# Optimization experiments

Hardware: AMD Instinct MI355X
Metric: run time of the kernel (lower is better)

Reference implementation:

```python
import jax, jax.numpy as jnp
import numpy as np

D, B, N, DIM, H, DH, MLP = 6, 4, 1024, 768, 12, 64, 3072
SCALE = DH ** -0.5
EPS = 1e-5


def setup_inputs() -> dict:
    key = jax.random.key(0)
    ks = jax.random.split(key, 5)
    s = 0.02
    return {
        "x": jax.random.normal(ks[0], (B, N, DIM), jnp.float32),
        "ln1_g": jnp.ones((D, DIM), jnp.float32),
        "ln1_b": jnp.zeros((D, DIM), jnp.float32),
        "wqkv": jax.random.normal(ks[1], (D, DIM, 3 * H * DH), jnp.float32) * s,
        "wo": jax.random.normal(ks[2], (D, H * DH, DIM), jnp.float32) * s,
        "bo": jnp.zeros((D, DIM), jnp.float32),
        "ln2_g": jnp.ones((D, DIM), jnp.float32),
        "ln2_b": jnp.zeros((D, DIM), jnp.float32),
        "w1": jax.random.normal(ks[3], (D, DIM, MLP), jnp.float32) * s,
        "b1": jnp.zeros((D, MLP), jnp.float32),
        "w2": jax.random.normal(ks[4], (D, MLP, DIM), jnp.float32) * s,
        "b2": jnp.zeros((D, DIM), jnp.float32),
    }


def _ln(h, g, b):
    m = h.mean(-1, keepdims=True)
    v = h.var(-1, keepdims=True)  # biased, matches torch LayerNorm
    return (h - m) / jnp.sqrt(v + EPS) * g + b


def _heads(t):
    # [b, n, h*d] -> [b, h, n, d]
    return t.reshape(B, N, H, DH).transpose(0, 2, 1, 3)


def reference(x, ln1_g, ln1_b, wqkv, wo, bo, ln2_g, ln2_b, w1, b1, w2, b2):
    def step(carry, p):
        xc, _, _ = carry
        g1, be1, Wqkv, Wo, Bo, g2, be2, W1, B1, W2, B2 = p
        h = _ln(xc, g1, be1)
        q, k, v = jnp.split(h @ Wqkv, 3, axis=-1)
        q, k, v = _heads(q), _heads(k), _heads(v)
        attn = jax.nn.softmax(jnp.einsum('bhid,bhjd->bhij', q, k) * SCALE, axis=-1)
        out = jnp.einsum('bhij,bhjd->bhid', attn, v)
        out = out.transpose(0, 2, 1, 3).reshape(B, N, H * DH)
        xc = xc + out @ Wo + Bo
        h2 = _ln(xc, g2, be2)
        xc = xc + jax.nn.gelu(h2 @ W1 + B1, approximate=False) @ W2 + B2
        return (xc, k, v), None

    kv0 = jnp.zeros((B, H, N, DH), x.dtype)
    (xf, k, v), _ = jax.lax.scan(
        step, (x, kv0, kv0),
        (ln1_g, ln1_b, wqkv, wo, bo, ln2_g, ln2_b, w1, b1, w2, b2))
    return xf, k, v
```

## Files before the change

### kernel.cpp

```cpp
#include <hip/hip_runtime.h>
#include <hip/hip_bf16.h>
#include <math.h>

typedef __bf16 bf16;
typedef __bf16 bf16x8 __attribute__((ext_vector_type(8)));
typedef float f32x4 __attribute__((ext_vector_type(4)));

enum { EPI_QKV = 0, EPI_GELU = 1 };

__device__ __forceinline__ void gload16(const void* g, void* s) {
  __builtin_amdgcn_global_load_lds((__attribute__((address_space(1))) void*)g,
                                   (__attribute__((address_space(3))) void*)s, 16, 0, 0);
}

#define MFMA16(a, b, c) __builtin_amdgcn_mfma_f32_16x16x32_bf16((a), (b), (c), 0, 0, 0)

__device__ __forceinline__ void xcd_swizzle(int& bx, int& by) {
  const int gx = gridDim.x, nwg = gx * gridDim.y;
  int bid = blockIdx.y * gx + blockIdx.x;
  if ((nwg & 7) == 0) bid = (bid & 7) * (nwg >> 3) + (bid >> 3);
  bx = bid % gx;
  by = bid / gx;
}

__global__ __launch_bounds__(256) void cast_x(const float* __restrict__ x,
                                              float* __restrict__ xq) {
  const int i = (blockIdx.x * 256 + threadIdx.x) * 4;
  float4 v = *(const float4*)(x + i);
  v.x = (float)(bf16)v.x; v.y = (float)(bf16)v.y;
  v.z = (float)(bf16)v.z; v.w = (float)(bf16)v.w;
  *(float4*)(xq + i) = v;
}

__global__ __launch_bounds__(256) void wconv_all(
    const float* __restrict__ wqkv, const float* __restrict__ wo,
    const float* __restrict__ w1, const float* __restrict__ w2,
    bf16* __restrict__ qkvT, bf16* __restrict__ woT,
    bf16* __restrict__ w1T, bf16* __restrict__ w2T, int lfix) {
  __shared__ float tile[64][65];
  const int bid = blockIdx.x, t = threadIdx.x;
  int l, r;
  if (lfix < 0) { l = bid / 1728; r = bid % 1728; } else { l = lfix; r = bid; }
  const int lo = (lfix < 0) ? l : 0;
  const float* W; bf16* Wt; int K, N, tt;
  if (r < 432)       { W = wqkv + (size_t)l * 768 * 2304; Wt = qkvT + (size_t)lo * 2304 * 768; K = 768;  N = 2304; tt = r; }
  else if (r < 576)  { W = wo   + (size_t)l * 768 * 768;  Wt = woT  + (size_t)lo * 768 * 768;  K = 768;  N = 768;  tt = r - 432; }
  else if (r < 1152) { W = w1   + (size_t)l * 768 * 3072; Wt = w1T  + (size_t)lo * 3072 * 768; K = 768;  N = 3072; tt = r - 576; }
  else               { W = w2   + (size_t)l * 3072 * 768; Wt = w2T  + (size_t)lo * 768 * 3072; K = 3072; N = 768;  tt = r - 1152; }
  const int ntx = N >> 6;
  const int n0 = (tt % ntx) * 64, k0 = (tt / ntx) * 64;
  const int tx = t & 63, ty = t >> 6;
#pragma unroll
  for (int rr = 0; rr < 16; ++rr) {
    const int row = ty + rr * 4;
    tile[row][tx] = W[(size_t)(k0 + row) * N + n0 + tx];
  }
  __syncthreads();
#pragma unroll
  for (int it = 0; it < 2; ++it) {
    const int c = it * 256 + t;
    const int n = c >> 3, kc = (c & 7) * 8;
    bf16x8 v;
#pragma unroll
    for (int j = 0; j < 8; ++j) v[j] = (bf16)tile[kc + j][n];
    *(bf16x8*)(Wt + (size_t)(n0 + n) * K + k0 + kc) = v;
  }
}

__global__ __launch_bounds__(256) void ln_kernel(const float* __restrict__ x,
                                                 const float* __restrict__ g,
                                                 const float* __restrict__ b,
                                                 bf16* __restrict__ out) {
  const int row = blockIdx.x, t = threadIdx.x;
  const float* xr = x + (size_t)row * 768;
  float v0 = xr[t], v1 = xr[t + 256], v2 = xr[t + 512];
  float s = v0 + v1 + v2, sq = v0 * v0 + v1 * v1 + v2 * v2;
#pragma unroll
  for (int m = 32; m; m >>= 1) { s += __shfl_xor(s, m); sq += __shfl_xor(sq, m); }
  __shared__ float rs[4], rq[4];
  const int w = t >> 6;
  if ((t & 63) == 0) { rs[w] = s; rq[w] = sq; }
  __syncthreads();
  s = rs[0] + rs[1] + rs[2] + rs[3];
  sq = rq[0] + rq[1] + rq[2] + rq[3];
  const float mean = s * (1.f / 768.f);
  const float var = sq * (1.f / 768.f) - mean * mean;
  const float rstd = rsqrtf(var + 1e-5f);
  bf16* orow = out + (size_t)row * 768;
  orow[t]       = (bf16)((v0 - mean) * rstd * g[t]       + b[t]);
  orow[t + 256] = (bf16)((v1 - mean) * rstd * g[t + 256] + b[t + 256]);
  orow[t + 512] = (bf16)((v2 - mean) * rstd * g[t + 512] + b[t + 512]);
}

template <int EPI>
__global__ __launch_bounds__(256) void gemm_s(
    const bf16* __restrict__ A, const bf16* __restrict__ Bt,
    const float* __restrict__ bias, bf16* __restrict__ Cb,
    bf16* __restrict__ qo, bf16* __restrict__ ko_, bf16* __restrict__ vo,
    float* __restrict__ kf, float* __restrict__ vf, int wf,
    int M, int Nc, int K) {
  __shared__ __align__(16) char lds[2][2][8192];
  const int t = threadIdx.x, lane = t & 63, w = t >> 6;
  const int wr = w >> 1, wc = w & 1;
  int bx, by;
  xcd_swizzle(bx, by);
  const size_t m0 = (size_t)by * 128, n0 = (size_t)bx * 128;

  const char* ab[2]; const char* bb[2];
#pragma unroll
  for (int r = 0; r < 2; ++r) {
    int c = r * 256 + t;
    ab[r] = (const char*)(A + (m0 + (c >> 2)) * (size_t)K) + (c & 3) * 16;
    bb[r] = (const char*)(Bt + (n0 + (c >> 2)) * (size_t)K) + (c & 3) * 16;
  }

  f32x4 acc[4][4] = {};

  auto stage = [&](int buf, int tt) {
#pragma unroll
    for (int r = 0; r < 2; ++r) {
      gload16(ab[r] + (size_t)tt * 64, &lds[buf][0][r * 4096 + w * 1024]);
      gload16(bb[r] + (size_t)tt * 64, &lds[buf][1][r * 4096 + w * 1024]);
    }
  };
  auto compute = [&](int buf) {
    const char* As = lds[buf][0];
    const char* Bs = lds[buf][1];
    const int ko = (lane >> 4) * 16;
    bf16x8 af[4], fb[4];
#pragma unroll
    for (int i = 0; i < 4; ++i) {
      af[i] = *(const bf16x8*)(As + (wr * 64 + i * 16 + (lane & 15)) * 64 + ko);
      fb[i] = *(const bf16x8*)(Bs + (wc * 64 + i * 16 + (lane & 15)) * 64 + ko);
    }
#pragma unroll
    for (int mi = 0; mi < 4; ++mi)
#pragma unroll
      for (int ni = 0; ni < 4; ++ni)
        acc[mi][ni] = MFMA16(af[mi], fb[ni], acc[mi][ni]);
  };

  const int NT = K >> 5;
  stage(0, 0);
  __syncthreads();
  int cur = 0;
  for (int tt = 1; tt < NT; ++tt) {
    stage(cur ^ 1, tt);
    compute(cur);
    __syncthreads();
    cur ^= 1;
  }
  compute(cur);

#pragma unroll
  for (int mi = 0; mi < 4; ++mi) {
#pragma unroll
    for (int i = 0; i < 4; ++i) {
      size_t row = m0 + wr * 64 + mi * 16 + ((lane >> 4) << 2) + i;
#pragma unroll
      for (int ni = 0; ni < 4; ++ni) {
        size_t col = n0 + wc * 64 + ni * 16 + (lane & 15);
        float v = acc[mi][ni][i];
        if (EPI == EPI_GELU) {
          v += bias[col];
          v = 0.5f * v * (1.f + erff(v * 0.70710678118f));
          Cb[row * (size_t)Nc + col] = (bf16)v;
        } else {
          int b = (int)(row >> 10), n = (int)(row & 1023);
          int which = (int)col >= 1536 ? 2 : ((int)col >= 768 ? 1 : 0);
          int hd = (int)col - which * 768;
          int hh = hd >> 6, d = hd & 63;
          size_t dst = ((size_t)(b * 12 + hh) * 1024 + n) * 64 + d;
          if (which == 0) {
            qo[dst] = (bf16)(v * 0.125f);
          } else if (which == 1) {
            ko_[dst] = (bf16)v;
            if (wf) kf[dst] = v;
          } else {
            vo[dst] = (bf16)v;
            if (wf) vf[dst] = v;
          }
        }
      }
    }
  }
}

__global__ __launch_bounds__(256) void gemm64_s(
    const bf16* __restrict__ A, const bf16* __restrict__ Bt,
    const float* __restrict__ bias, const float* __restrict__ res,
    float* __restrict__ Cf, int M, int Nc, int K) {
  __shared__ __align__(16) char lds[2][12288];
  const int t = threadIdx.x, lane = t & 63, w = t >> 6;
  const int wr = w >> 1, wc = w & 1;
  const int l15 = lane & 15, l4 = lane >> 4;
  int bx, by;
  xcd_swizzle(bx, by);
  const size_t m0 = (size_t)by * 64, n0 = (size_t)bx * 128;

  const char* ab = (const char*)(A + (m0 + (t >> 2)) * (size_t)K) + (t & 3) * 16;
  const char* b0 = (const char*)(Bt + (n0 + (t >> 2)) * (size_t)K) + (t & 3) * 16;
  const char* b1 = (const char*)(Bt + (n0 + 64 + (t >> 2)) * (size_t)K) + (t & 3) * 16;

  f32x4 acc[2][4] = {};

  auto stage = [&](int buf, int tt) {
    gload16(ab + (size_t)tt * 64, &lds[buf][t * 16]);
    gload16(b0 + (size_t)tt * 64, &lds[buf][4096 + t * 16]);
    gload16(b1 + (size_t)tt * 64, &lds[buf][8192 + t * 16]);
  };
  auto compute = [&](int buf) {
    const char* L = lds[buf];
    const int ko = l4 * 16;
    bf16x8 fa[2], fb[4];
#pragma unroll
    for (int mi = 0; mi < 2; ++mi)
      fa[mi] = *(const bf16x8*)(L + (wr * 32 + mi * 16 + l15) * 64 + ko);
#pragma unroll
    for (int ni = 0; ni < 4; ++ni)
      fb[ni] = *(const bf16x8*)(L + 4096 + (wc * 64 + ni * 16 + l15) * 64 + ko);
#pragma unroll
    for (int mi = 0; mi < 2; ++mi)
#pragma unroll
      for (int ni = 0; ni < 4; ++ni)
        acc[mi][ni] = MFMA16(fa[mi], fb[ni], acc[mi][ni]);
  };

  const int NT = K >> 5;
  stage(0, 0);
  __syncthreads();
  int cur = 0;
  for (int tt = 1; tt < NT; ++tt) {
    stage(cur ^ 1, tt);
    compute(cur);
    __syncthreads();
    cur ^= 1;
  }
  compute(cur);

#pragma unroll
  for (int mi = 0; mi < 2; ++mi) {
#pragma unroll
    for (int i = 0; i < 4; ++i) {
      size_t row = m0 + wr * 32 + mi * 16 + l4 * 4 + i;
#pragma unroll
      for (int ni = 0; ni < 4; ++ni) {
        size_t col = n0 + wc * 64 + ni * 16 + l15;
        float v = acc[mi][ni][i] + bias[col] + res[row * (size_t)Nc + col];
        Cf[row * (size_t)Nc + col] = v;
      }
    }
  }
}

__global__ __launch_bounds__(256) void vtrans(const bf16* __restrict__ v,
                                              bf16* __restrict__ vT) {
  __shared__ bf16 tile[32][33];
  const int tx = threadIdx.x, ty = threadIdx.y;
  const int bh = blockIdx.x, n0 = blockIdx.y * 32, d0 = blockIdx.z * 32;
  const bf16* vb = v + (size_t)bh * 1024 * 64;
  bf16* vTb = vT + (size_t)bh * 64 * 1024;
#pragma unroll
  for (int r = 0; r < 4; ++r)
    tile[ty + r * 8][tx] = vb[(size_t)(n0 + ty + r * 8) * 64 + d0 + tx];
  __syncthreads();
#pragma unroll
  for (int r = 0; r < 4; ++r)
    vTb[(size_t)(d0 + ty + r * 8) * 1024 + n0 + tx] = tile[tx][ty + r * 8];
}

__global__ __launch_bounds__(64) void attn_kernel(const bf16* __restrict__ q,
                                                  const bf16* __restrict__ k,
                                                  const bf16* __restrict__ vT,
                                                  bf16* __restrict__ out) {
  __shared__ __align__(16) char Ks[16384];
  __shared__ __align__(16) char Vs[16384];
  char* Ps = Ks;
  const int bh = blockIdx.x, qb = blockIdx.y;
  const int lane = threadIdx.x & 63;
  const int l15 = lane & 15, l4 = lane >> 4;

  const char* kp = (const char*)(k + (size_t)bh * 1024 * 64);
  const char* vp = (const char*)(vT + (size_t)bh * 64 * 1024);

  const char* kb0 = kp + (lane >> 3) * 128 + (((lane & 7) ^ ((lane >> 3) & 7)) * 16);
  const int vr0 = lane >> 4;
  const char* vb0 = vp + (size_t)vr0 * 2048 + (((lane & 15) ^ vr0) * 16);
  const char* vb1 = vp + (size_t)(vr0 + 4) * 2048 + (((lane & 15) ^ (vr0 + 4)) * 16);

  bf16x8 aq[2][2];
  {
    const bf16* qbase = q + ((size_t)bh * 1024 + qb * 32) * 64;
#pragma unroll
    for (int mi = 0; mi < 2; ++mi)
#pragma unroll
      for (int ks = 0; ks < 2; ++ks)
        aq[mi][ks] = *(const bf16x8*)(qbase + (mi * 16 + l15) * 64 + ks * 32 + l4 * 8);
  }

  f32x4 oacc[2][4] = {};
  float mrun[2][4], lrun[2][4];
#pragma unroll
  for (int mi = 0; mi < 2; ++mi)
#pragma unroll
    for (int i = 0; i < 4; ++i) { mrun[mi][i] = -1e30f; lrun[mi][i] = 0.f; }

  for (int kb = 0; kb < 8; ++kb) {
    const char* ksrc = kb0 + (size_t)kb * 16384;
#pragma unroll
    for (int r = 0; r < 16; ++r)
      gload16(ksrc + r * 1024, &Ks[r * 1024]);
    const char* vsrc0 = vb0 + kb * 256;
    const char* vsrc1 = vb1 + kb * 256;
#pragma unroll
    for (int r = 0; r < 8; ++r) {
      gload16(vsrc0 + (size_t)r * 16384, &Vs[r * 2048]);
      gload16(vsrc1 + (size_t)r * 16384, &Vs[r * 2048 + 1024]);
    }
    asm volatile("s_waitcnt vmcnt(16)" ::: "memory");
    __builtin_amdgcn_sched_barrier(0);

    f32x4 sacc[2][8] = {};
#pragma unroll
    for (int ks = 0; ks < 2; ++ks) {
#pragma unroll
      for (int ni = 0; ni < 8; ++ni) {
        const int rr = ni * 16 + l15;
        const bf16x8 bk = *(const bf16x8*)(Ks + rr * 128 + (((ks * 4 + l4) ^ (rr & 7)) * 16));
        sacc[0][ni] = MFMA16(aq[0][ks], bk, sacc[0][ni]);
        sacc[1][ni] = MFMA16(aq[1][ks], bk, sacc[1][ni]);
      }
    }

#pragma unroll
    for (int mi = 0; mi < 2; ++mi) {
#pragma unroll
      for (int i = 0; i < 4; ++i) {
        float mx = sacc[mi][0][i];
#pragma unroll
        for (int ni = 1; ni < 8; ++ni) mx = fmaxf(mx, sacc[mi][ni][i]);
#pragma unroll
        for (int sh = 8; sh; sh >>= 1) mx = fmaxf(mx, __shfl_xor(mx, sh));
        float mnew = fmaxf(mrun[mi][i], mx);
        float alpha = __expf(mrun[mi][i] - mnew);
        mrun[mi][i] = mnew;
        float rsum = 0.f;
#pragma unroll
        for (int ni = 0; ni < 8; ++ni) {
          float pe = __expf(sacc[mi][ni][i] - mnew);
          sacc[mi][ni][i] = pe;
          rsum += pe;
        }
#pragma unroll
        for (int sh = 8; sh; sh >>= 1) rsum += __shfl_xor(rsum, sh);
        lrun[mi][i] = lrun[mi][i] * alpha + rsum;
#pragma unroll
        for (int ni = 0; ni < 4; ++ni) oacc[mi][ni][i] *= alpha;
      }
    }

#pragma unroll
    for (int mi = 0; mi < 2; ++mi)
#pragma unroll
      for (int i = 0; i < 4; ++i) {
        int rowl = mi * 16 + l4 * 4 + i;
        char* prp = Ps + rowl * 256;
        int sw = rowl & 7;
#pragma unroll
        for (int ni = 0; ni < 8; ++ni) {
          int col = ni * 16 + l15;
          *(bf16*)(prp + (((col >> 3) ^ sw) * 16) + (col & 7) * 2) = (bf16)sacc[mi][ni][i];
        }
      }

    asm volatile("s_waitcnt vmcnt(0)" ::: "memory");
    __builtin_amdgcn_sched_barrier(0);

    const int prow0 = l15, prow1 = 16 + l15;
#pragma unroll
    for (int ks = 0; ks < 4; ++ks) {
      const bf16x8 ap0 = *(const bf16x8*)(Ps + prow0 * 256 + (((ks * 4 + l4) ^ (prow0 & 7)) * 16));
      const bf16x8 ap1 = *(const bf16x8*)(Ps + prow1 * 256 + (((ks * 4 + l4) ^ (prow1 & 7)) * 16));
#pragma unroll
      for (int ni = 0; ni < 4; ++ni) {
        const int vr = ni * 16 + l15;
        const bf16x8 bv = *(const bf16x8*)(Vs + vr * 256 + (((ks * 4 + l4) ^ (vr & 7)) * 16));
        oacc[0][ni] = MFMA16(ap0, bv, oacc[0][ni]);
        oacc[1][ni] = MFMA16(ap1, bv, oacc[1][ni]);
      }
    }
  }

  const int b = bh / 12, hh = bh % 12;
#pragma unroll
  for (int mi = 0; mi < 2; ++mi)
#pragma unroll
    for (int i = 0; i < 4; ++i) {
      int n = qb * 32 + mi * 16 + l4 * 4 + i;
      float inv = 1.f / lrun[mi][i];
      bf16* orow = out + ((size_t)b * 1024 + n) * 768 + hh * 64;
#pragma unroll
      for (int ni = 0; ni < 4; ++ni)
        orow[ni * 16 + l15] = (bf16)(oacc[mi][ni][i] * inv);
    }
}

extern "C" void kernel_launch(void* const* d_in, const int* in_sizes, int n_in,
                              void* d_out, int out_size, void* d_ws, size_t ws_size,
                              hipStream_t stream) {
  (void)in_sizes; (void)n_in; (void)out_size;
  const float* x_in = (const float*)d_in[0];
  const float* ln1g = (const float*)d_in[1];
  const float* ln1b = (const float*)d_in[2];
  const float* wqkv = (const float*)d_in[3];
  const float* wo   = (const float*)d_in[4];
  const float* bo   = (const float*)d_in[5];
  const float* ln2g = (const float*)d_in[6];
  const float* ln2b = (const float*)d_in[7];
  const float* w1   = (const float*)d_in[8];
  const float* b1   = (const float*)d_in[9];
  const float* w2   = (const float*)d_in[10];
  const float* b2   = (const float*)d_in[11];

  float* outx = (float*)d_out;
  float* outk = outx + (size_t)4096 * 768;
  float* outv = outk + (size_t)4096 * 768;

  char* p = (char*)d_ws;
  auto take = [&](size_t bytes) {
    char* r = p;
    p += (bytes + 255) & ~(size_t)255;
    return r;
  };
  float* xw   = (float*)take((size_t)4096 * 768 * 4);
  bf16*  h    = (bf16*)take((size_t)4096 * 768 * 2);
  bf16*  mbuf = (bf16*)take((size_t)4096 * 3072 * 2);
  bf16*  qbuf = (bf16*)take((size_t)4096 * 768 * 2);
  bf16*  kbuf = (bf16*)take((size_t)4096 * 768 * 2);
  bf16*  vbuf = (bf16*)take((size_t)4096 * 768 * 2);
  bf16*  vTb  = (bf16*)take((size_t)4096 * 768 * 2);
  bf16*  abuf = (bf16*)take((size_t)4096 * 768 * 2);

  const size_t wq1 = (size_t)2304 * 768, wo1 = (size_t)768 * 768,
               w11 = (size_t)3072 * 768, w21 = (size_t)768 * 3072;
  const size_t used = (size_t)(p - (char*)d_ws);
  const size_t wbytes = (wq1 + wo1 + w11 + w21) * 2;
  const bool hoist = ws_size >= used + 6 * wbytes + 8192;
  const int nl = hoist ? 6 : 1;
  bf16* qkvT = (bf16*)take(wq1 * 2 * nl);
  bf16* woT  = (bf16*)take(wo1 * 2 * nl);
  bf16* w1T  = (bf16*)take(w11 * 2 * nl);
  bf16* w2T  = (bf16*)take(w21 * 2 * nl);

  cast_x<<<3072, 256, 0, stream>>>(x_in, xw);
  if (hoist)
    wconv_all<<<10368, 256, 0, stream>>>(wqkv, wo, w1, w2, qkvT, woT, w1T, w2T, -1);

  for (int l = 0; l < 6; ++l) {
    if (!hoist)
      wconv_all<<<1728, 256, 0, stream>>>(wqkv, wo, w1, w2, qkvT, woT, w1T, w2T, l);
    bf16* qkL = qkvT + (hoist ? (size_t)l * wq1 : 0);
    bf16* woL = woT  + (hoist ? (size_t)l * wo1 : 0);
    bf16* w1L = w1T  + (hoist ? (size_t)l * w11 : 0);
    bf16* w2L = w2T  + (hoist ? (size_t)l * w21 : 0);

    ln_kernel<<<4096, 256, 0, stream>>>(xw, ln1g + l * 768, ln1b + l * 768, h);
    gemm_s<EPI_QKV><<<dim3(18, 32), 256, 0, stream>>>(
        h, qkL, nullptr, nullptr, qbuf, kbuf, vbuf, outk, outv, l == 5 ? 1 : 0,
        4096, 2304, 768);
    vtrans<<<dim3(48, 32, 2), dim3(32, 8), 0, stream>>>(vbuf, vTb);
    attn_kernel<<<dim3(48, 32), 64, 0, stream>>>(qbuf, kbuf, vTb, abuf);
    gemm64_s<<<dim3(6, 64), 256, 0, stream>>>(
        abuf, woL, bo + l * 768, xw, xw, 4096, 768, 768);
    ln_kernel<<<4096, 256, 0, stream>>>(xw, ln2g + l * 768, ln2b + l * 768, h);
    gemm_s<EPI_GELU><<<dim3(24, 32), 256, 0, stream>>>(
        h, w1L, b1 + l * 3072, mbuf, nullptr, nullptr, nullptr, nullptr, nullptr, 0,
        4096, 3072, 768);
    gemm64_s<<<dim3(6, 64), 256, 0, stream>>>(
        mbuf, w2L, b2 + l * 768, xw, (l == 5) ? outx : xw, 4096, 768, 3072);
  }
}
```

Measured before the change: 1.294 ms.

## Compute softmax row sums via MFMA with ones vector; vectorize weight conversion loads

The attention kernel no longer accumulates softmax row sums with scalar adds and cross-lane shuffles. It instead runs an extra MFMA of the bf16 probability tile against a vector of ones into a separate accumulator, rescaled by alpha alongside the output. This removes shuffle and VALU work from the softmax but adds two MFMAs per k-step and makes the denominator use bf16-rounded probabilities. Separately, the weight-conversion transpose kernel now loads float4 per thread instead of scalar floats.

```diff
diff --git a/kernel.cpp b/kernel.cpp
--- a/kernel.cpp
+++ b/kernel.cpp
@@ -49,11 +49,13 @@
   else               { W = w2   + (size_t)l * 3072 * 768; Wt = w2T  + (size_t)lo * 768 * 3072; K = 3072; N = 768;  tt = r - 1152; }
   const int ntx = N >> 6;
   const int n0 = (tt % ntx) * 64, k0 = (tt / ntx) * 64;
-  const int tx = t & 63, ty = t >> 6;
-#pragma unroll
-  for (int rr = 0; rr < 16; ++rr) {
-    const int row = ty + rr * 4;
-    tile[row][tx] = W[(size_t)(k0 + row) * N + n0 + tx];
+  const int cx = (t & 15) * 4, ry = t >> 4;
+#pragma unroll
+  for (int pp = 0; pp < 4; ++pp) {
+    const int row = ry + pp * 16;
+    const float4 v = *(const float4*)(W + (size_t)(k0 + row) * N + n0 + cx);
+    tile[row][cx] = v.x; tile[row][cx + 1] = v.y;
+    tile[row][cx + 2] = v.z; tile[row][cx + 3] = v.w;
   }
   __syncthreads();
 #pragma unroll
@@ -298,12 +300,17 @@
         aq[mi][ks] = *(const bf16x8*)(qbase + (mi * 16 + l15) * 64 + ks * 32 + l4 * 8);
   }
 
+  bf16x8 vones;
+#pragma unroll
+  for (int j = 0; j < 8; ++j) vones[j] = (bf16)1.0f;
+
   f32x4 oacc[2][4] = {};
-  float mrun[2][4], lrun[2][4];
+  f32x4 lacc[2] = {};
+  float mrun[2][4];
 #pragma unroll
   for (int mi = 0; mi < 2; ++mi)
 #pragma unroll
-    for (int i = 0; i < 4; ++i) { mrun[mi][i] = -1e30f; lrun[mi][i] = 0.f; }
+    for (int i = 0; i < 4; ++i) mrun[mi][i] = -1e30f;
 
   for (int kb = 0; kb < 8; ++kb) {
     const char* ksrc = kb0 + (size_t)kb * 16384;
@@ -344,18 +351,12 @@
         float mnew = fmaxf(mrun[mi][i], mx);
         float alpha = __expf(mrun[mi][i] - mnew);
         mrun[mi][i] = mnew;
-        float rsum = 0.f;
-#pragma unroll
-        for (int ni = 0; ni < 8; ++ni) {
-          float pe = __expf(sacc[mi][ni][i] - mnew);
-          sacc[mi][ni][i] = pe;
-          rsum += pe;
-        }
-#pragma unroll
-        for (int sh = 8; sh; sh >>= 1) rsum += __shfl_xor(rsum, sh);
-        lrun[mi][i] = lrun[mi][i] * alpha + rsum;
+#pragma unroll
+        for (int ni = 0; ni < 8; ++ni)
+          sacc[mi][ni][i] = __expf(sacc[mi][ni][i] - mnew);
 #pragma unroll
         for (int ni = 0; ni < 4; ++ni) oacc[mi][ni][i] *= alpha;
+        lacc[mi][i] *= alpha;
       }
     }
 
@@ -388,6 +389,8 @@
         oacc[0][ni] = MFMA16(ap0, bv, oacc[0][ni]);
         oacc[1][ni] = MFMA16(ap1, bv, oacc[1][ni]);
       }
+      lacc[0] = MFMA16(ap0, vones, lacc[0]);
+      lacc[1] = MFMA16(ap1, vones, lacc[1]);
     }
   }
 
@@ -397,7 +400,7 @@
 #pragma unroll
     for (int i = 0; i < 4; ++i) {
       int n = qb * 32 + mi * 16 + l4 * 4 + i;
-      float inv = 1.f / lrun[mi][i];
+      float inv = 1.f / lacc[mi][i];
       bf16* orow = out + ((size_t)b * 1024 + n) * 768 + hh * 64;
 #pragma unroll
       for (int ni = 0; ni < 4; ++ni)
```

After: 1.270 ms. About the same (-1.9%).
